# Kernel tuning notes

Hardware: AMD Instinct MI355X
Metric: run time of the kernel (lower is better)

## Reference

```python
import jax, jax.numpy as jnp
import numpy as np


def setup_inputs() -> dict:
    key = jax.random.key(0)
    k1, k2, k3, k4 = jax.random.split(key, 4)
    B, D, N, M = 4, 256, 4096, 4096
    return {
        "src": jax.random.normal(k1, (B, 3, N), dtype=jnp.float32),
        "tgt": jax.random.normal(k2, (B, 3, M), dtype=jnp.float32),
        "src_emb": jax.random.normal(k3, (B, D, N), dtype=jnp.float32),
        "tgt_emb": jax.random.normal(k4, (B, D, M), dtype=jnp.float32),
    }


def reference(src, tgt, src_emb, tgt_emb):
    # pairwise_distance[b,n,m] = -||src_emb[:,n] - tgt_emb[:,m]||^2
    # decomposed as -xx + 2*inner - yy (inner below is -2*dot, as in torch code)
    inner = -2.0 * jnp.einsum("bdn,bdm->bnm", src_emb, tgt_emb)       # [B,N,M]
    xx = jnp.sum(src_emb ** 2, axis=1)[:, :, None]                     # [B,N,1]
    yy = jnp.sum(tgt_emb ** 2, axis=1)[:, None, :]                     # [B,1,M]
    pairwise_distance = -xx - inner - yy                               # [B,N,M]
    scores = jax.nn.softmax(pairwise_distance, axis=2)                 # softmax over tgt points
    # src_corr[b,c,n] = sum_m tgt[b,c,m] * scores[b,n,m]
    src_corr = jnp.einsum("bcm,bnm->bcn", tgt, scores)                 # [B,3,N]
    return src_corr
```

## Files before the change

### kernel.cpp

```cpp
#include <hip/hip_runtime.h>

#define NBATCH 4
#define DDIM   256
#define NN     4096
#define MM     4096
#define NCHUNK 8
#define MCHUNK 512
#define MTILE  64
#define NT     (MCHUNK / MTILE)
#define LOG2E  1.44269504088896340736f

using half8   = __attribute__((ext_vector_type(8))) _Float16;
using floatx4 = __attribute__((ext_vector_type(4))) float;

__global__ __launch_bounds__(256) void k_prep(const float* __restrict__ src_emb,
                                              const float* __restrict__ tgt_emb,
                                              const float* __restrict__ tgt,
                                              _Float16* __restrict__ Qh,
                                              _Float16* __restrict__ Kh,
                                              float* __restrict__ yyS,
                                              float4* __restrict__ Vt) {
    __shared__ float tile[64][257];
    __shared__ float psum[8][64];
    int bz = blockIdx.z, tensor = bz >> 2, b = bz & 3;
    const float* in = tensor ? tgt_emb : src_emb;
    _Float16* out = tensor ? Kh : Qh;
    const float scale = tensor ? 1.0f : 2.0f * LOG2E;
    int n0 = blockIdx.x * 64;
    int t = threadIdx.x;

    int c2 = t & 31, part = t >> 5;
    const float* ip = in + (size_t)(b * DDIM + part) * NN + n0 + c2 * 2;
    float s0 = 0.f, s1 = 0.f;
#pragma unroll
    for (int i = 0; i < 32; i++) {
        float2 v = *(const float2*)(ip + (size_t)(i * 8) * NN);
        tile[c2 * 2][part + i * 8]     = v.x;
        tile[c2 * 2 + 1][part + i * 8] = v.y;
        s0 = fmaf(v.x, v.x, s0);
        s1 = fmaf(v.y, v.y, s1);
    }
    if (tensor) { psum[part][c2 * 2] = s0; psum[part][c2 * 2 + 1] = s1; }
    __syncthreads();

    int dg = t & 31, nn = t >> 5;
#pragma unroll
    for (int p = 0; p < 8; p++) {
        int n = p * 8 + nn;
        const float* row = &tile[n][dg * 8];
        half8 h;
#pragma unroll
        for (int k = 0; k < 8; k++) h[k] = (_Float16)(row[k] * scale);
        *(half8*)(out + (size_t)(b * NN + n0 + n) * DDIM + dg * 8) = h;
    }
    if (tensor && t < 64) {
        float s = 0.f;
#pragma unroll
        for (int j = 0; j < 8; j++) s += psum[j][t];
        int m = n0 + t;
        yyS[b * MM + m] = s * (-LOG2E);
        Vt[(size_t)b * MM + m] = make_float4(tgt[(size_t)b * 3 * MM + m],
                                             tgt[(size_t)b * 3 * MM + MM + m],
                                             tgt[(size_t)b * 3 * MM + 2 * MM + m], 1.0f);
    }
}

__global__ __launch_bounds__(256, 2) void k_flash(const _Float16* __restrict__ Qh,
                                                  const _Float16* __restrict__ Kh,
                                                  const float* __restrict__ yyS,
                                                  const float4* __restrict__ Vt,
                                                  float4* __restrict__ Opart,
                                                  float* __restrict__ Mpart) {
    __shared__ __align__(16) _Float16 Kt[2][MTILE * DDIM];

    int i = blockIdx.x;
    int xcd = i & 7, sb = i >> 3;
    int grp = xcd + 8 * (sb >> 4);
    int b = grp >> 3, chunk = grp & 7, ntile = sb & 15;

    int t = threadIdx.x, wave = t >> 6, lane = t & 63, quad = lane >> 4, l15 = lane & 15;
    int n0 = ntile * 256 + wave * 64;
    int m0 = chunk * MCHUNK;

    const half8* qp = (const half8*)Qh + (size_t)b * NN * 32;
    half8 qf[4][8];
#pragma unroll
    for (int nb = 0; nb < 4; nb++) {
        int n = n0 + nb * 16 + l15;
#pragma unroll
        for (int ds = 0; ds < 8; ds++) qf[nb][ds] = qp[n * 32 + ds * 4 + quad];
    }

    const _Float16* kp = Kh + (size_t)b * MM * DDIM;
    int ssl = lane & 31, shalf = lane >> 5;
    auto stage = [&](int mt) {
        const _Float16* gb = kp + (size_t)(m0 + mt * MTILE + wave * 16) * DDIM;
        _Float16* lb = &Kt[mt & 1][wave * 16 * DDIM];
#pragma unroll
        for (int it = 0; it < 8; it++) {
            int rl = it * 2 + shalf;
            int rloc = wave * 16 + rl;
            int g = (ssl & 24) | ((ssl ^ rloc) & 7);
            const _Float16* gp = gb + (size_t)rl * DDIM + g * 8;
            __builtin_amdgcn_global_load_lds(
                (const __attribute__((address_space(1))) uint32_t*)(const void*)gp,
                (__attribute__((address_space(3))) uint32_t*)(void*)(lb + it * 2 * DDIM),
                16, 0, 0);
        }
    };

    const floatx4 z4 = {0.f, 0.f, 0.f, 0.f};
    floatx4 o[4] = {z4, z4, z4, z4};
    float mr[4];
#pragma unroll
    for (int nb = 0; nb < 4; nb++) mr[nb] = -__builtin_inff();

    const float* yb = yyS + (size_t)b * MM;
    const float4* vb = Vt + (size_t)b * MM;
    int r7 = l15 & 7;

    stage(0);
    for (int mt = 0; mt < NT; mt++) {
        __syncthreads();

        int jb = m0 + mt * MTILE + quad * 4;
        floatx4 yv[4];
#pragma unroll
        for (int mb = 0; mb < 4; mb++) yv[mb] = *(const floatx4*)(yb + jb + mb * 16);

        if (mt + 1 < NT) stage(mt + 1);

        const _Float16* Kb = &Kt[mt & 1][0];
        floatx4 acc[4][4];
#pragma unroll
        for (int nb = 0; nb < 4; nb++)
#pragma unroll
            for (int mb = 0; mb < 4; mb++) acc[nb][mb] = z4;

#pragma unroll
        for (int ds = 0; ds < 8; ds++) {
            int slot = (ds * 4 + quad) ^ r7;
            half8 a[4];
#pragma unroll
            for (int mb = 0; mb < 4; mb++)
                a[mb] = *(const half8*)(Kb + (size_t)(mb * 16 + l15) * DDIM + slot * 8);
#pragma unroll
            for (int nb = 0; nb < 4; nb++)
#pragma unroll
                for (int mb = 0; mb < 4; mb++)
                    acc[nb][mb] = __builtin_amdgcn_mfma_f32_16x16x32_f16(a[mb], qf[nb][ds], acc[nb][mb], 0, 0, 0);
        }

#pragma unroll
        for (int nb = 0; nb < 4; nb++) {
#pragma unroll
            for (int mb = 0; mb < 4; mb++) acc[nb][mb] = acc[nb][mb] + yv[mb];
            floatx4 mx = __builtin_elementwise_max(
                __builtin_elementwise_max(acc[nb][0], acc[nb][1]),
                __builtin_elementwise_max(acc[nb][2], acc[nb][3]));
            float tm = fmaxf(fmaxf(mx[0], mx[1]), fmaxf(mx[2], mx[3]));
            float mn = fmaxf(mr[nb], tm);
            float al = __builtin_amdgcn_exp2f(mr[nb] - mn);
            mr[nb] = mn;
            o[nb] = o[nb] * al;
            floatx4 mnv = {mn, mn, mn, mn};
#pragma unroll
            for (int mb = 0; mb < 4; mb++) acc[nb][mb] = acc[nb][mb] - mnv;
        }
#pragma unroll
        for (int mb = 0; mb < 4; mb++) {
            const float4* vp = vb + jb + mb * 16;
            float4 v0 = vp[0], v1 = vp[1], v2 = vp[2], v3 = vp[3];
#pragma unroll
            for (int nb = 0; nb < 4; nb++) {
                floatx4 pa;
#pragma unroll
                for (int r = 0; r < 4; r++) pa[r] = __builtin_amdgcn_exp2f(acc[nb][mb][r]);
                floatx4 oo = o[nb];
                oo += pa[0] * (floatx4){v0.x, v0.y, v0.z, v0.w};
                oo += pa[1] * (floatx4){v1.x, v1.y, v1.z, v1.w};
                oo += pa[2] * (floatx4){v2.x, v2.y, v2.z, v2.w};
                oo += pa[3] * (floatx4){v3.x, v3.y, v3.z, v3.w};
                o[nb] = oo;
            }
        }
    }

#pragma unroll
    for (int nb = 0; nb < 4; nb++) {
        float mq = mr[nb];
        float ma = fmaxf(mq, __shfl_xor(mq, 16, 64));
        ma = fmaxf(ma, __shfl_xor(ma, 32, 64));
        float w = __builtin_amdgcn_exp2f(mq - ma);
        floatx4 ow = o[nb] * w;
#pragma unroll
        for (int c = 0; c < 4; c++) {
            float v = ow[c];
            v += __shfl_xor(v, 16, 64);
            v += __shfl_xor(v, 32, 64);
            ow[c] = v;
        }
        o[nb] = ow;
        mr[nb] = ma;
    }
    if (quad == 0) {
#pragma unroll
        for (int nb = 0; nb < 4; nb++) {
            int n = n0 + nb * 16 + l15;
            size_t idx = (size_t)(chunk * NBATCH + b) * NN + n;
            Opart[idx] = make_float4(o[nb][0], o[nb][1], o[nb][2], o[nb][3]);
            Mpart[idx] = mr[nb];
        }
    }
}

__global__ __launch_bounds__(128) void k_combine(const float4* __restrict__ Opart,
                                                 const float* __restrict__ Mpart,
                                                 float* __restrict__ out) {
    int idx = blockIdx.x * 128 + threadIdx.x;
    int b = idx >> 12, n = idx & (NN - 1);
    float mstar = -__builtin_inff();
#pragma unroll
    for (int j = 0; j < NCHUNK; j++)
        mstar = fmaxf(mstar, Mpart[(size_t)(j * NBATCH + b) * NN + n]);
    float o0 = 0.f, o1 = 0.f, o2 = 0.f, l = 0.f;
#pragma unroll
    for (int j = 0; j < NCHUNK; j++) {
        size_t id = (size_t)(j * NBATCH + b) * NN + n;
        float w = __builtin_amdgcn_exp2f(Mpart[id] - mstar);
        float4 P = Opart[id];
        o0 = fmaf(w, P.x, o0); o1 = fmaf(w, P.y, o1);
        o2 = fmaf(w, P.z, o2); l  = fmaf(w, P.w, l);
    }
    out[(size_t)(b * 3 + 0) * NN + n] = o0 / l;
    out[(size_t)(b * 3 + 1) * NN + n] = o1 / l;
    out[(size_t)(b * 3 + 2) * NN + n] = o2 / l;
}

extern "C" void kernel_launch(void* const* d_in, const int* in_sizes, int n_in,
                              void* d_out, int out_size, void* d_ws, size_t ws_size,
                              hipStream_t stream) {
    const float* tgt     = (const float*)d_in[1];
    const float* src_emb = (const float*)d_in[2];
    const float* tgt_emb = (const float*)d_in[3];
    float* out = (float*)d_out;

    char* ws = (char*)d_ws;
    _Float16* Qh  = (_Float16*)(ws);
    _Float16* Kh  = (_Float16*)(ws + 8388608);
    float*    yyS = (float*)   (ws + 16777216);
    float4*   Vt  = (float4*)  (ws + 16842752);
    float4*   Op  = (float4*)  (ws + 17104896);
    float*    Mp  = (float*)   (ws + 19202048);

    hipLaunchKernelGGL(k_prep,    dim3(64, 1, 8), dim3(256), 0, stream,
                       src_emb, tgt_emb, tgt, Qh, Kh, yyS, Vt);
    hipLaunchKernelGGL(k_flash,   dim3(512),      dim3(256), 0, stream, Qh, Kh, yyS, Vt, Op, Mp);
    hipLaunchKernelGGL(k_combine, dim3(128),      dim3(128), 0, stream, Op, Mp, out);
}
```

Before: 148.4 us.

## Pre-swizzle Q/K into MFMA fragment layout and read K directly from global

The prep kernel now writes Q and K in a blocked layout that matches the MFMA fragment order, so each lane's half8 operands are contiguous. The flash kernel drops the LDS double-buffered K staging and loads K fragments straight from global/L2 into registers. It caches V and yy for its chunk in LDS instead. It also halves the rows per wave (2 n-blocks instead of 4), doubles the grid to 1024 blocks and raises the occupancy hint to 3 blocks per CU, trading K reuse across rows for more parallelism and no barriers. The risk is more global/L2 traffic for K, since each K tile is now read per wave rather than shared through LDS.

```diff
diff --git a/kernel.cpp b/kernel.cpp
--- a/kernel.cpp
+++ b/kernel.cpp
@@ -6,155 +6,133 @@
 #define MM     4096
 #define NCHUNK 8
 #define MCHUNK 512
-#define MTILE  64
-#define NT     (MCHUNK / MTILE)
 #define LOG2E  1.44269504088896340736f
 
 using half8   = __attribute__((ext_vector_type(8))) _Float16;
 using floatx4 = __attribute__((ext_vector_type(4))) float;
+
 
 __global__ __launch_bounds__(256) void k_prep(const float* __restrict__ src_emb,
                                               const float* __restrict__ tgt_emb,
                                               const float* __restrict__ tgt,
-                                              _Float16* __restrict__ Qh,
-                                              _Float16* __restrict__ Kh,
+                                              _Float16* __restrict__ Qf,
+                                              _Float16* __restrict__ Kf,
                                               float* __restrict__ yyS,
                                               float4* __restrict__ Vt) {
-    __shared__ float tile[64][257];
-    __shared__ float psum[8][64];
-    int bz = blockIdx.z, tensor = bz >> 2, b = bz & 3;
+    __shared__ float psum[4][64];
+    int i = blockIdx.x;
+    int xcd = i & 7, j = i >> 3;
+    int b = xcd >> 1, nhalf = xcd & 1;
+    int tensor = j & 1, sub = j >> 1;
+    int n0 = nhalf * 2048 + sub * 64;
     const float* in = tensor ? tgt_emb : src_emb;
-    _Float16* out = tensor ? Kh : Qh;
+    _Float16* outp  = tensor ? Kf : Qf;
     const float scale = tensor ? 1.0f : 2.0f * LOG2E;
-    int n0 = blockIdx.x * 64;
-    int t = threadIdx.x;
-
-    int c2 = t & 31, part = t >> 5;
-    const float* ip = in + (size_t)(b * DDIM + part) * NN + n0 + c2 * 2;
-    float s0 = 0.f, s1 = 0.f;
-#pragma unroll
-    for (int i = 0; i < 32; i++) {
-        float2 v = *(const float2*)(ip + (size_t)(i * 8) * NN);
-        tile[c2 * 2][part + i * 8]     = v.x;
-        tile[c2 * 2 + 1][part + i * 8] = v.y;
-        s0 = fmaf(v.x, v.x, s0);
-        s1 = fmaf(v.y, v.y, s1);
-    }
-    if (tensor) { psum[part][c2 * 2] = s0; psum[part][c2 * 2 + 1] = s1; }
+    int t = threadIdx.x, w = t >> 6, ln = t & 63;
+    const float* ib = in + (size_t)b * DDIM * NN + n0 + ln;
+    _Float16* ob = outp + (size_t)b * NN * 32 * 8;
+    int blk = (n0 + ln) >> 4, l15 = ln & 15;
+    float ss = 0.f;
+#pragma unroll
+    for (int h = 0; h < 2; h++) {
+        int ds = w + h * 4;
+#pragma unroll
+        for (int oct = 0; oct < 4; oct++) {
+            half8 v;
+#pragma unroll
+            for (int k = 0; k < 8; k++) {
+                float f = ib[(size_t)(ds * 32 + oct * 8 + k) * NN];
+                ss = fmaf(f, f, ss);
+                v[k] = (_Float16)(f * scale);
+            }
+            *(half8*)(ob + ((((size_t)blk * 8 + ds) * 4 + oct) * 16 + l15) * 8) = v;
+        }
+    }
+    if (tensor) psum[w][ln] = ss;
     __syncthreads();
-
-    int dg = t & 31, nn = t >> 5;
-#pragma unroll
-    for (int p = 0; p < 8; p++) {
-        int n = p * 8 + nn;
-        const float* row = &tile[n][dg * 8];
-        half8 h;
-#pragma unroll
-        for (int k = 0; k < 8; k++) h[k] = (_Float16)(row[k] * scale);
-        *(half8*)(out + (size_t)(b * NN + n0 + n) * DDIM + dg * 8) = h;
-    }
-    if (tensor && t < 64) {
-        float s = 0.f;
-#pragma unroll
-        for (int j = 0; j < 8; j++) s += psum[j][t];
-        int m = n0 + t;
-        yyS[b * MM + m] = s * (-LOG2E);
-        Vt[(size_t)b * MM + m] = make_float4(tgt[(size_t)b * 3 * MM + m],
-                                             tgt[(size_t)b * 3 * MM + MM + m],
-                                             tgt[(size_t)b * 3 * MM + 2 * MM + m], 1.0f);
-    }
-}
-
-__global__ __launch_bounds__(256, 2) void k_flash(const _Float16* __restrict__ Qh,
-                                                  const _Float16* __restrict__ Kh,
+    if (tensor) {
+        if (t < 64) {
+            float s = psum[0][t] + psum[1][t] + psum[2][t] + psum[3][t];
+            yyS[b * MM + n0 + t] = s * (-LOG2E);
+        } else if (t < 128) {
+            int m = n0 + (t - 64);
+            const float* tp = tgt + (size_t)b * 3 * MM + m;
+            Vt[(size_t)b * MM + m] = make_float4(tp[0], tp[MM], tp[2 * MM], 1.0f);
+        }
+    }
+}
+
+__global__ __launch_bounds__(256, 3) void k_flash(const _Float16* __restrict__ Qf,
+                                                  const _Float16* __restrict__ Kf,
                                                   const float* __restrict__ yyS,
                                                   const float4* __restrict__ Vt,
                                                   float4* __restrict__ Opart,
                                                   float* __restrict__ Mpart) {
-    __shared__ __align__(16) _Float16 Kt[2][MTILE * DDIM];
-
-    int i = blockIdx.x;
-    int xcd = i & 7, sb = i >> 3;
-    int grp = xcd + 8 * (sb >> 4);
-    int b = grp >> 3, chunk = grp & 7, ntile = sb & 15;
-
-    int t = threadIdx.x, wave = t >> 6, lane = t & 63, quad = lane >> 4, l15 = lane & 15;
-    int n0 = ntile * 256 + wave * 64;
+    __shared__ floatx4 vtt[MCHUNK];
+    __shared__ floatx4 yyt[MCHUNK / 4];
+
+    int i = blockIdx.x, t = threadIdx.x;
+    int xcd = i & 7, j = i >> 3;
+    int b = xcd >> 1, nhalf = xcd & 1;
+    int chunk = j & 7, ntile = nhalf * 16 + (j >> 3);
+
+    int wave = t >> 6, lane = t & 63, quad = lane >> 4, l15 = lane & 15;
     int m0 = chunk * MCHUNK;
 
-    const half8* qp = (const half8*)Qh + (size_t)b * NN * 32;
-    half8 qf[4][8];
-#pragma unroll
-    for (int nb = 0; nb < 4; nb++) {
-        int n = n0 + nb * 16 + l15;
-#pragma unroll
-        for (int ds = 0; ds < 8; ds++) qf[nb][ds] = qp[n * 32 + ds * 4 + quad];
-    }
-
-    const _Float16* kp = Kh + (size_t)b * MM * DDIM;
-    int ssl = lane & 31, shalf = lane >> 5;
-    auto stage = [&](int mt) {
-        const _Float16* gb = kp + (size_t)(m0 + mt * MTILE + wave * 16) * DDIM;
-        _Float16* lb = &Kt[mt & 1][wave * 16 * DDIM];
-#pragma unroll
-        for (int it = 0; it < 8; it++) {
-            int rl = it * 2 + shalf;
-            int rloc = wave * 16 + rl;
-            int g = (ssl & 24) | ((ssl ^ rloc) & 7);
-            const _Float16* gp = gb + (size_t)rl * DDIM + g * 8;
-            __builtin_amdgcn_global_load_lds(
-                (const __attribute__((address_space(1))) uint32_t*)(const void*)gp,
-                (__attribute__((address_space(3))) uint32_t*)(void*)(lb + it * 2 * DDIM),
-                16, 0, 0);
-        }
-    };
+    {
+        const float4* vb = Vt + (size_t)b * MM + m0;
+        for (int r = t; r < MCHUNK; r += 256) {
+            float4 g = vb[r];
+            vtt[r] = (floatx4){g.x, g.y, g.z, g.w};
+        }
+        const floatx4* yb = (const floatx4*)(yyS + (size_t)b * MM + m0);
+        for (int r = t; r < MCHUNK / 4; r += 256) yyt[r] = yb[r];
+    }
+
+    int nblk0 = ntile * 8 + wave * 2;
+    const half8* qp = (const half8*)Qf + (size_t)b * NN * 32;
+    half8 qf[2][8];
+#pragma unroll
+    for (int nb = 0; nb < 2; nb++)
+#pragma unroll
+        for (int ds = 0; ds < 8; ds++)
+            qf[nb][ds] = qp[(((size_t)(nblk0 + nb) * 8 + ds) * 4 + quad) * 16 + l15];
+
+    const half8* kp = (const half8*)Kf + (size_t)b * NN * 32;
 
     const floatx4 z4 = {0.f, 0.f, 0.f, 0.f};
-    floatx4 o[4] = {z4, z4, z4, z4};
-    float mr[4];
-#pragma unroll
-    for (int nb = 0; nb < 4; nb++) mr[nb] = -__builtin_inff();
-
-    const float* yb = yyS + (size_t)b * MM;
-    const float4* vb = Vt + (size_t)b * MM;
-    int r7 = l15 & 7;
-
-    stage(0);
-    for (int mt = 0; mt < NT; mt++) {
-        __syncthreads();
-
-        int jb = m0 + mt * MTILE + quad * 4;
-        floatx4 yv[4];
-#pragma unroll
-        for (int mb = 0; mb < 4; mb++) yv[mb] = *(const floatx4*)(yb + jb + mb * 16);
-
-        if (mt + 1 < NT) stage(mt + 1);
-
-        const _Float16* Kb = &Kt[mt & 1][0];
-        floatx4 acc[4][4];
-#pragma unroll
-        for (int nb = 0; nb < 4; nb++)
+    floatx4 o[2] = {z4, z4};
+    float mr[2] = {-__builtin_inff(), -__builtin_inff()};
+
+    __syncthreads();
+
+    for (int mt = 0; mt < MCHUNK / 64; mt++) {
+        int mblk0 = chunk * 32 + mt * 4;
+
+        half8 a[4][8];
+#pragma unroll
+        for (int mb = 0; mb < 4; mb++)
+#pragma unroll
+            for (int ds = 0; ds < 8; ds++)
+                a[mb][ds] = kp[(((size_t)(mblk0 + mb) * 8 + ds) * 4 + quad) * 16 + l15];
+
+        floatx4 acc[2][4];
+#pragma unroll
+        for (int nb = 0; nb < 2; nb++)
 #pragma unroll
             for (int mb = 0; mb < 4; mb++) acc[nb][mb] = z4;
-
-#pragma unroll
-        for (int ds = 0; ds < 8; ds++) {
-            int slot = (ds * 4 + quad) ^ r7;
-            half8 a[4];
-#pragma unroll
-            for (int mb = 0; mb < 4; mb++)
-                a[mb] = *(const half8*)(Kb + (size_t)(mb * 16 + l15) * DDIM + slot * 8);
-#pragma unroll
-            for (int nb = 0; nb < 4; nb++)
+#pragma unroll
+        for (int ds = 0; ds < 8; ds++)
+#pragma unroll
+            for (int nb = 0; nb < 2; nb++)
 #pragma unroll
                 for (int mb = 0; mb < 4; mb++)
-                    acc[nb][mb] = __builtin_amdgcn_mfma_f32_16x16x32_f16(a[mb], qf[nb][ds], acc[nb][mb], 0, 0, 0);
-        }
-
-#pragma unroll
-        for (int nb = 0; nb < 4; nb++) {
-#pragma unroll
-            for (int mb = 0; mb < 4; mb++) acc[nb][mb] = acc[nb][mb] + yv[mb];
+                    acc[nb][mb] = __builtin_amdgcn_mfma_f32_16x16x32_f16(a[mb][ds], qf[nb][ds], acc[nb][mb], 0, 0, 0);
+
+#pragma unroll
+        for (int nb = 0; nb < 2; nb++) {
+#pragma unroll
+            for (int mb = 0; mb < 4; mb++) acc[nb][mb] = acc[nb][mb] + yyt[mt * 16 + mb * 4 + quad];
             floatx4 mx = __builtin_elementwise_max(
                 __builtin_elementwise_max(acc[nb][0], acc[nb][1]),
                 __builtin_elementwise_max(acc[nb][2], acc[nb][3]));
@@ -169,30 +147,26 @@
         }
 #pragma unroll
         for (int mb = 0; mb < 4; mb++) {
-            const float4* vp = vb + jb + mb * 16;
-            float4 v0 = vp[0], v1 = vp[1], v2 = vp[2], v3 = vp[3];
-#pragma unroll
-            for (int nb = 0; nb < 4; nb++) {
-                floatx4 pa;
-#pragma unroll
-                for (int r = 0; r < 4; r++) pa[r] = __builtin_amdgcn_exp2f(acc[nb][mb][r]);
-                floatx4 oo = o[nb];
-                oo += pa[0] * (floatx4){v0.x, v0.y, v0.z, v0.w};
-                oo += pa[1] * (floatx4){v1.x, v1.y, v1.z, v1.w};
-                oo += pa[2] * (floatx4){v2.x, v2.y, v2.z, v2.w};
-                oo += pa[3] * (floatx4){v3.x, v3.y, v3.z, v3.w};
-                o[nb] = oo;
-            }
-        }
-    }
-
-#pragma unroll
-    for (int nb = 0; nb < 4; nb++) {
+            floatx4 vr[4];
+#pragma unroll
+            for (int r = 0; r < 4; r++) vr[r] = vtt[mt * 64 + mb * 16 + quad * 4 + r];
+#pragma unroll
+            for (int nb = 0; nb < 2; nb++)
+#pragma unroll
+                for (int r = 0; r < 4; r++) {
+                    float p = __builtin_amdgcn_exp2f(acc[nb][mb][r]);
+                    o[nb] = o[nb] + p * vr[r];
+                }
+        }
+    }
+
+#pragma unroll
+    for (int nb = 0; nb < 2; nb++) {
         float mq = mr[nb];
         float ma = fmaxf(mq, __shfl_xor(mq, 16, 64));
         ma = fmaxf(ma, __shfl_xor(ma, 32, 64));
-        float w = __builtin_amdgcn_exp2f(mq - ma);
-        floatx4 ow = o[nb] * w;
+        float wgt = __builtin_amdgcn_exp2f(mq - ma);
+        floatx4 ow = o[nb] * wgt;
 #pragma unroll
         for (int c = 0; c < 4; c++) {
             float v = ow[c];
@@ -200,16 +174,11 @@
             v += __shfl_xor(v, 32, 64);
             ow[c] = v;
         }
-        o[nb] = ow;
-        mr[nb] = ma;
-    }
-    if (quad == 0) {
-#pragma unroll
-        for (int nb = 0; nb < 4; nb++) {
-            int n = n0 + nb * 16 + l15;
+        if (quad == 0) {
+            int n = (nblk0 + nb) * 16 + l15;
             size_t idx = (size_t)(chunk * NBATCH + b) * NN + n;
-            Opart[idx] = make_float4(o[nb][0], o[nb][1], o[nb][2], o[nb][3]);
-            Mpart[idx] = mr[nb];
+            Opart[idx] = make_float4(ow[0], ow[1], ow[2], ow[3]);
+            Mpart[idx] = ma;
         }
     }
 }
@@ -246,15 +215,15 @@
     float* out = (float*)d_out;
 
     char* ws = (char*)d_ws;
-    _Float16* Qh  = (_Float16*)(ws);
-    _Float16* Kh  = (_Float16*)(ws + 8388608);
+    _Float16* Qf  = (_Float16*)(ws);
+    _Float16* Kf  = (_Float16*)(ws + 8388608);
     float*    yyS = (float*)   (ws + 16777216);
     float4*   Vt  = (float4*)  (ws + 16842752);
     float4*   Op  = (float4*)  (ws + 17104896);
     float*    Mp  = (float*)   (ws + 19202048);
 
-    hipLaunchKernelGGL(k_prep,    dim3(64, 1, 8), dim3(256), 0, stream,
-                       src_emb, tgt_emb, tgt, Qh, Kh, yyS, Vt);
-    hipLaunchKernelGGL(k_flash,   dim3(512),      dim3(256), 0, stream, Qh, Kh, yyS, Vt, Op, Mp);
-    hipLaunchKernelGGL(k_combine, dim3(128),      dim3(128), 0, stream, Op, Mp, out);
-}
+    hipLaunchKernelGGL(k_prep,    dim3(512),  dim3(256), 0, stream,
+                       src_emb, tgt_emb, tgt, Qf, Kf, yyS, Vt);
+    hipLaunchKernelGGL(k_flash,   dim3(1024), dim3(256), 0, stream, Qf, Kf, yyS, Vt, Op, Mp);
+    hipLaunchKernelGGL(k_combine, dim3(128),  dim3(128), 0, stream, Op, Mp, out);
+}
```

After: 231.0 us. 55.6% more time.
